# Kernel optimization log

Hardware: AMD Instinct MI355X
Metric: run time of the kernel (lower is better)

## Reference

```python
import jax, jax.numpy as jnp
import numpy as np

GROUPS = 4
KLD_SCALE = 10.0
COMMITMENT_COST = 0.25


def setup_inputs() -> dict:
    key = jax.random.key(0)
    k1, k2 = jax.random.split(key)
    z = jax.random.normal(k1, (8, 4096, 512), dtype=jnp.float32)
    embed_w = jax.random.normal(k2, (512, 128), dtype=jnp.float32)
    return {"z": z, "embed_w": embed_w}


def reference(z, embed_w):
    B, N, D = z.shape
    d = D // GROUPS  # sub-vector dim per group
    flat = z.reshape(B * N * GROUPS, d)  # [M, d]
    # squared euclidean distance to each codebook entry: [M, K]
    dist = (
        jnp.sum(flat * flat, axis=1, keepdims=True)
        - 2.0 * flat @ embed_w.T
        + jnp.sum(embed_w * embed_w, axis=1)[None, :]
    )
    ind = jnp.argmin(dist, axis=1)  # argmax(-dist)
    z_q = embed_w[ind]  # [M, d] codebook gather
    sg = jax.lax.stop_gradient
    diff = KLD_SCALE * (
        COMMITMENT_COST * jnp.mean((sg(z_q) - flat) ** 2)
        + jnp.mean((z_q - sg(flat)) ** 2)
    )
    # straight-through estimator
    z_q_st = (flat + sg(z_q - flat)).reshape(B, N, D)
    ind_out = ind.reshape(N, B, GROUPS)  # matches torch .view on contiguous buffer
    return (z_q_st, diff, ind_out)
```

## Files before the change

kernel.cpp:

```cpp
#include <hip/hip_runtime.h>
#include <float.h>


typedef _Float16 half8 __attribute__((ext_vector_type(8)));
typedef __attribute__((ext_vector_type(4))) float f32x4;

constexpr int Dn = 128;
constexpr int K  = 512;
constexpr long long Mrows = 131072;
constexpr int RPW   = 32;
constexpr int WAVES = 16;
constexpr int RPB   = RPW * WAVES;
constexpr int NBLK  = (int)(Mrows / RPB);
constexpr float TAU_A = 0.05f;

constexpr size_t ZQ_SIZE  = (size_t)Mrows * Dn;
constexpr size_t DIFF_OFF = ZQ_SIZE;
constexpr size_t IND_OFF  = ZQ_SIZE + 1;

__device__ inline void gload_lds16(const void* g, void* l) {
    __builtin_amdgcn_global_load_lds(
        (const __attribute__((address_space(1))) unsigned int*)g,
        (__attribute__((address_space(3))) unsigned int*)l,
        16, 0, 0);
}

__global__ void prep_kernel(const float* __restrict__ W,
                            unsigned short* __restrict__ Wp,
                            float* __restrict__ wn2,
                            double* __restrict__ wn64) {
    int t = blockIdx.x * 256 + threadIdx.x;
    int code = t >> 4;
    int g    = t & 15;
    const float* src = W + (size_t)code * Dn + g * 8;
    float4 a = *(const float4*)src;
    float4 b = *(const float4*)(src + 4);
    float vv[8] = {a.x, a.y, a.z, a.w, b.x, b.y, b.z, b.w};
    half8 hv;
    double s2 = 0.0;
    #pragma unroll
    for (int j = 0; j < 8; ++j) {
        hv[j] = (_Float16)vv[j];
        s2 += (double)vv[j] * (double)vv[j];
    }
    *(half8*)((char*)Wp + (size_t)code * 256 + ((g ^ (code & 7)) << 4)) = hv;
    s2 += __shfl_xor(s2, 1);
    s2 += __shfl_xor(s2, 2);
    s2 += __shfl_xor(s2, 4);
    s2 += __shfl_xor(s2, 8);
    if (g == 0) {
        wn2[code]  = (float)(-0.5 * s2);
        wn64[code] = s2;
    }
}

__global__ __launch_bounds__(1024, 4) void vq_main(
        const float* __restrict__ Z, const float* __restrict__ W,
        const unsigned short* __restrict__ Wp, const float* __restrict__ wn2,
        const double* __restrict__ wn64,
        float* __restrict__ out, double* __restrict__ diffsum) {
    __shared__ __align__(16) char Wlds[131072];
    __shared__ float wn2_s[K];
    __shared__ float xn_s[RPB];
    __shared__ int   sIdx[RPB];
    __shared__ int   flagList[RPB];
    __shared__ int   flagN;
    __shared__ float wpart[WAVES];

    const int tid  = threadIdx.x;
    const int w    = tid >> 6;
    const int lane = tid & 63;
    const int lm   = lane & 15;
    const int lg   = lane >> 4;
    const size_t row0 = (size_t)blockIdx.x * RPB;

    if (tid == 0) flagN = 0;

    {
        const char* gsrc = (const char*)Wp;
        #pragma unroll
        for (int it = 0; it < 8; ++it) {
            const int gbase = it * 1024 + w * 64;
            gload_lds16(gsrc + (size_t)(gbase + lane) * 16, Wlds + (size_t)gbase * 16);
        }
    }
    if (tid < K) wn2_s[tid] = wn2[tid];

    half8 ah[2][4];
    #pragma unroll
    for (int r = 0; r < 2; ++r) {
        const size_t grow = row0 + (size_t)w * RPW + r * 16 + lm;
        float s2 = 0.f;
        #pragma unroll
        for (int ks = 0; ks < 4; ++ks) {
            const float* xp = Z + grow * Dn + ks * 32 + lg * 8;
            float4 x0 = *(const float4*)xp;
            float4 x1 = *(const float4*)(xp + 4);
            float xv[8] = {x0.x, x0.y, x0.z, x0.w, x1.x, x1.y, x1.z, x1.w};
            #pragma unroll
            for (int j = 0; j < 8; ++j) {
                ah[r][ks][j] = (_Float16)xv[j];
                s2 += xv[j] * xv[j];
            }
        }
        s2 += __shfl_xor(s2, 16);
        s2 += __shfl_xor(s2, 32);
        if (lg == 0) xn_s[w * RPW + r * 16 + lm] = s2;
    }

    float m1[2][4], m2[2][4];
    int   i1[2][4];
    #pragma unroll
    for (int r = 0; r < 2; ++r)
        #pragma unroll
        for (int j = 0; j < 4; ++j) { m1[r][j] = -FLT_MAX; m2[r][j] = -FLT_MAX; i1[r][j] = 0; }

    asm volatile("s_waitcnt vmcnt(0)" ::: "memory");
    __syncthreads();

    const int t0 = (w * 2) & 31;
    #pragma unroll 2
    for (int ti = 0; ti < 32; ++ti) {
        const int t = (ti + t0) & 31;
        const int code = t * 16 + lm;
        const float cinit = wn2_s[code];
        half8 bh[4];
        #pragma unroll
        for (int ks = 0; ks < 4; ++ks) {
            const int off = code * 256 + ((((ks << 2) + lg) ^ (code & 7)) << 4);
            bh[ks] = *(const half8*)(Wlds + off);
        }
        f32x4 acc[2];
        #pragma unroll
        for (int r = 0; r < 2; ++r) acc[r] = (f32x4){cinit, cinit, cinit, cinit};
        #pragma unroll
        for (int ks = 0; ks < 4; ++ks) {
            #pragma unroll
            for (int r = 0; r < 2; ++r)
                acc[r] = __builtin_amdgcn_mfma_f32_16x16x32_f16(ah[r][ks], bh[ks], acc[r], 0, 0, 0);
        }
        #pragma unroll
        for (int r = 0; r < 2; ++r) {
            #pragma unroll
            for (int j = 0; j < 4; ++j) {
                const float a = acc[r][j];
                m2[r][j] = __builtin_amdgcn_fmed3f(a, m1[r][j], m2[r][j]);
                const bool gt = a > m1[r][j];
                m1[r][j] = fmaxf(m1[r][j], a);
                i1[r][j] = gt ? code : i1[r][j];
            }
        }
    }

    #pragma unroll
    for (int sft = 1; sft < 16; sft <<= 1) {
        #pragma unroll
        for (int r = 0; r < 2; ++r) {
            #pragma unroll
            for (int j = 0; j < 4; ++j) {
                float o1 = __shfl_xor(m1[r][j], sft);
                float o2 = __shfl_xor(m2[r][j], sft);
                int   oi = __shfl_xor(i1[r][j], sft);
                if (o1 > m1[r][j] || (o1 == m1[r][j] && oi < i1[r][j])) {
                    m2[r][j] = fmaxf(m1[r][j], o2);
                    m1[r][j] = o1;
                    i1[r][j] = oi;
                } else {
                    m2[r][j] = fmaxf(m2[r][j], o1);
                }
            }
        }
    }

    float psum = 0.f;
    if (lm == 0) {
        #pragma unroll
        for (int r = 0; r < 2; ++r) {
            #pragma unroll
            for (int j = 0; j < 4; ++j) {
                const int row = w * RPW + r * 16 + lg * 4 + j;
                sIdx[row] = i1[r][j];
                psum += xn_s[row] - 2.f * m1[r][j];
                if (m1[r][j] - m2[r][j] < TAU_A) {
                    int pos = atomicAdd(&flagN, 1);
                    flagList[pos] = row;
                }
            }
        }
    }
    __syncthreads();

    {
        const int nf = flagN;
        const int cg    = lane >> 3;
        const int dbase = (lane & 7) * 16;
        for (int fi = w; fi < nf; fi += WAVES) {
            const int rr = flagList[fi];
            const float* xp = Z + (row0 + rr) * Dn + dbase;
            double xd[16];
            #pragma unroll
            for (int q = 0; q < 16; q += 4) {
                float4 v = *(const float4*)(xp + q);
                xd[q] = v.x; xd[q+1] = v.y; xd[q+2] = v.z; xd[q+3] = v.w;
            }
            double best = 1e300; int bi = 0;
            for (int cb = 0; cb < 64; ++cb) {
                const int c = cb * 8 + cg;
                const float* wp = W + (size_t)c * Dn + dbase;
                double s = 0.0;
                #pragma unroll
                for (int q = 0; q < 16; q += 4) {
                    float4 wv = *(const float4*)(wp + q);
                    s += xd[q]   * (double)wv.x;
                    s += xd[q+1] * (double)wv.y;
                    s += xd[q+2] * (double)wv.z;
                    s += xd[q+3] * (double)wv.w;
                }
                s += __shfl_xor(s, 1);
                s += __shfl_xor(s, 2);
                s += __shfl_xor(s, 4);
                const double sc = wn64[c] - 2.0 * s;
                if (sc < best) { best = sc; bi = c; }
            }
            #pragma unroll
            for (int sft = 8; sft < 64; sft <<= 1) {
                double ob = __shfl_xor(best, sft);
                int    ok = __shfl_xor(bi, sft);
                if (ob < best || (ob == best && ok < bi)) { best = ob; bi = ok; }
            }
            if (lane == 0) sIdx[rr] = bi;
        }
    }
    __syncthreads();

    #pragma unroll
    for (int it = 0; it < 16; ++it) {
        int f4i = lane + it * 64;
        int rl  = f4i >> 5, cq = f4i & 31;
        int ind = sIdx[w * RPW + rl];
        float4 wv = ((const float4*)(W + (size_t)ind * Dn))[cq];
        ((float4*)(out + (row0 + w * RPW + rl) * Dn))[cq] = wv;
    }
    if (lane < RPW)
        out[IND_OFF + row0 + w * RPW + lane] = (float)sIdx[w * RPW + lane];

    #pragma unroll
    for (int sft = 1; sft < 64; sft <<= 1) psum += __shfl_xor(psum, sft);
    if (lane == 0) wpart[w] = psum;
    __syncthreads();
    if (tid == 0) {
        double t = 0.0;
        #pragma unroll
        for (int i = 0; i < WAVES; ++i) t += (double)wpart[i];
        atomicAdd(diffsum, t);
    }
}

__global__ void diff_kernel(const double* __restrict__ diffsum, float* __restrict__ out) {
    if (threadIdx.x == 0 && blockIdx.x == 0) {
        out[DIFF_OFF] = (float)(12.5 * diffsum[0] / (double)ZQ_SIZE);
    }
}

extern "C" void kernel_launch(void* const* d_in, const int* in_sizes, int n_in,
                              void* d_out, int out_size, void* d_ws, size_t ws_size,
                              hipStream_t stream) {
    (void)in_sizes; (void)n_in; (void)out_size; (void)ws_size;
    const float* Z = (const float*)d_in[0];
    const float* W = (const float*)d_in[1];
    float* out = (float*)d_out;
    double* diffsum = (double*)d_ws;
    float*  wn2  = (float*)((char*)d_ws + 64);
    double* wn64 = (double*)((char*)d_ws + 2112);
    unsigned short* Wp = (unsigned short*)((char*)d_ws + 8192);

    hipMemsetAsync(d_ws, 0, 16, stream);
    prep_kernel<<<32, 256, 0, stream>>>(W, Wp, wn2, wn64);
    vq_main<<<NBLK, 1024, 0, stream>>>(Z, W, Wp, wn2, wn64, out, diffsum);
    diff_kernel<<<1, 64, 0, stream>>>(diffsum, out);
}
```

Baseline: 113.8 us.

## Halve LDS codebook buffer and stream codebook in two staged halves

Shrinks blocks from 16 to 8 waves and replaces the full 128KB LDS codebook copy with a 64KB buffer that is filled twice, once per half of the codes, with barriers between halves. The goal is to cut per-block LDS so more blocks can be resident per CU and the codebook load is smaller per stage. In exchange it doubles the number of blocks, and so the total codebook traffic into LDS, and adds a mid-loop sync where the second half load is fully exposed rather than overlapped. It also drops the per-wave staggered start of the tile loop.

```diff
diff --git a/kernel.cpp b/kernel.cpp
--- a/kernel.cpp
+++ b/kernel.cpp
@@ -9,9 +9,10 @@
 constexpr int K  = 512;
 constexpr long long Mrows = 131072;
 constexpr int RPW   = 32;
-constexpr int WAVES = 16;
+constexpr int WAVES = 8;
 constexpr int RPB   = RPW * WAVES;
 constexpr int NBLK  = (int)(Mrows / RPB);
+constexpr int KHALF = 256;
 constexpr float TAU_A = 0.05f;
 
 constexpr size_t ZQ_SIZE  = (size_t)Mrows * Dn;
@@ -54,12 +55,12 @@
     }
 }
 
-__global__ __launch_bounds__(1024, 4) void vq_main(
+__global__ __launch_bounds__(512, 4) void vq_main(
         const float* __restrict__ Z, const float* __restrict__ W,
         const unsigned short* __restrict__ Wp, const float* __restrict__ wn2,
         const double* __restrict__ wn64,
         float* __restrict__ out, double* __restrict__ diffsum) {
-    __shared__ __align__(16) char Wlds[131072];
+    __shared__ __align__(16) char Wbuf[KHALF * 256];
     __shared__ float wn2_s[K];
     __shared__ float xn_s[RPB];
     __shared__ int   sIdx[RPB];
@@ -76,15 +77,15 @@
 
     if (tid == 0) flagN = 0;
 
-    {
-        const char* gsrc = (const char*)Wp;
+    auto stage = [&](int p) {
+        const char* gsrc = (const char*)Wp + (size_t)p * (KHALF * 256);
         #pragma unroll
         for (int it = 0; it < 8; ++it) {
-            const int gbase = it * 1024 + w * 64;
-            gload_lds16(gsrc + (size_t)(gbase + lane) * 16, Wlds + (size_t)gbase * 16);
-        }
-    }
-    if (tid < K) wn2_s[tid] = wn2[tid];
+            const int gbase = it * 512 + w * 64;
+            gload_lds16(gsrc + (size_t)(gbase + lane) * 16, Wbuf + (size_t)gbase * 16);
+        }
+    };
+    stage(0);
 
     half8 ah[2][4];
     #pragma unroll
@@ -107,6 +108,7 @@
         s2 += __shfl_xor(s2, 32);
         if (lg == 0) xn_s[w * RPW + r * 16 + lm] = s2;
     }
+    if (tid < K) wn2_s[tid] = wn2[tid];
 
     float m1[2][4], m2[2][4];
     int   i1[2][4];
@@ -118,37 +120,45 @@
     asm volatile("s_waitcnt vmcnt(0)" ::: "memory");
     __syncthreads();
 
-    const int t0 = (w * 2) & 31;
-    #pragma unroll 2
-    for (int ti = 0; ti < 32; ++ti) {
-        const int t = (ti + t0) & 31;
-        const int code = t * 16 + lm;
-        const float cinit = wn2_s[code];
-        half8 bh[4];
-        #pragma unroll
-        for (int ks = 0; ks < 4; ++ks) {
-            const int off = code * 256 + ((((ks << 2) + lg) ^ (code & 7)) << 4);
-            bh[ks] = *(const half8*)(Wlds + off);
-        }
-        f32x4 acc[2];
-        #pragma unroll
-        for (int r = 0; r < 2; ++r) acc[r] = (f32x4){cinit, cinit, cinit, cinit};
-        #pragma unroll
-        for (int ks = 0; ks < 4; ++ks) {
-            #pragma unroll
-            for (int r = 0; r < 2; ++r)
-                acc[r] = __builtin_amdgcn_mfma_f32_16x16x32_f16(ah[r][ks], bh[ks], acc[r], 0, 0, 0);
-        }
-        #pragma unroll
-        for (int r = 0; r < 2; ++r) {
-            #pragma unroll
-            for (int j = 0; j < 4; ++j) {
-                const float a = acc[r][j];
-                m2[r][j] = __builtin_amdgcn_fmed3f(a, m1[r][j], m2[r][j]);
-                const bool gt = a > m1[r][j];
-                m1[r][j] = fmaxf(m1[r][j], a);
-                i1[r][j] = gt ? code : i1[r][j];
-            }
+    for (int p = 0; p < 2; ++p) {
+        const int cbase = p * KHALF;
+        #pragma unroll 2
+        for (int t = 0; t < 16; ++t) {
+            const int code_l = t * 16 + lm;
+            const int code   = cbase + code_l;
+            const float cinit = wn2_s[code];
+            half8 bh[4];
+            #pragma unroll
+            for (int ks = 0; ks < 4; ++ks) {
+                const int off = code_l * 256 + ((((ks << 2) + lg) ^ (code_l & 7)) << 4);
+                bh[ks] = *(const half8*)(Wbuf + off);
+            }
+            f32x4 acc[2];
+            #pragma unroll
+            for (int r = 0; r < 2; ++r) acc[r] = (f32x4){cinit, cinit, cinit, cinit};
+            #pragma unroll
+            for (int ks = 0; ks < 4; ++ks) {
+                #pragma unroll
+                for (int r = 0; r < 2; ++r)
+                    acc[r] = __builtin_amdgcn_mfma_f32_16x16x32_f16(ah[r][ks], bh[ks], acc[r], 0, 0, 0);
+            }
+            #pragma unroll
+            for (int r = 0; r < 2; ++r) {
+                #pragma unroll
+                for (int j = 0; j < 4; ++j) {
+                    const float a = acc[r][j];
+                    m2[r][j] = __builtin_amdgcn_fmed3f(a, m1[r][j], m2[r][j]);
+                    const bool gt = a > m1[r][j];
+                    m1[r][j] = fmaxf(m1[r][j], a);
+                    i1[r][j] = gt ? code : i1[r][j];
+                }
+            }
+        }
+        if (p == 0) {
+            __syncthreads();
+            stage(1);
+            asm volatile("s_waitcnt vmcnt(0)" ::: "memory");
+            __syncthreads();
         }
     }
 
@@ -276,6 +286,6 @@
 
     hipMemsetAsync(d_ws, 0, 16, stream);
     prep_kernel<<<32, 256, 0, stream>>>(W, Wp, wn2, wn64);
-    vq_main<<<NBLK, 1024, 0, stream>>>(Z, W, Wp, wn2, wn64, out, diffsum);
+    vq_main<<<NBLK, 512, 0, stream>>>(Z, W, Wp, wn2, wn64, out, diffsum);
     diff_kernel<<<1, 64, 0, stream>>>(diffsum, out);
 }
```

After: 113.1 us. Within noise of the previous version (-0.6%).

## Split codebook gather into separate wide kernel and drop staggered tile order

Applied to the files above, without the earlier changes.

Moves the z_q gather and write out of the heavy 1024-thread scan kernel into a separate lightweight kernel with many small blocks. That kernel reads indices back from the output buffer and folds the final diff scalar write in through a last-block atomic counter. The intent is to keep the scan kernel's tail from serializing large stores and to spread the store traffic across more blocks. It also removes the per-wave rotated start of the codebook tile loop, which may increase LDS bank conflicts, and it adds an extra pass over the index data.

```diff
diff --git a/kernel.cpp b/kernel.cpp
--- a/kernel.cpp
+++ b/kernel.cpp
@@ -12,6 +12,8 @@
 constexpr int WAVES = 16;
 constexpr int RPB   = RPW * WAVES;
 constexpr int NBLK  = (int)(Mrows / RPB);
+constexpr int GROWS = 64;
+constexpr int NGBLK = (int)(Mrows / GROWS);
 constexpr float TAU_A = 0.05f;
 
 constexpr size_t ZQ_SIZE  = (size_t)Mrows * Dn;
@@ -54,7 +56,7 @@
     }
 }
 
-__global__ __launch_bounds__(1024, 4) void vq_main(
+__global__ __launch_bounds__(1024, 4) void vq_scan(
         const float* __restrict__ Z, const float* __restrict__ W,
         const unsigned short* __restrict__ Wp, const float* __restrict__ wn2,
         const double* __restrict__ wn64,
@@ -118,10 +120,8 @@
     asm volatile("s_waitcnt vmcnt(0)" ::: "memory");
     __syncthreads();
 
-    const int t0 = (w * 2) & 31;
     #pragma unroll 2
-    for (int ti = 0; ti < 32; ++ti) {
-        const int t = (ti + t0) & 31;
+    for (int t = 0; t < 32; ++t) {
         const int code = t * 16 + lm;
         const float cinit = wn2_s[code];
         half8 bh[4];
@@ -233,16 +233,7 @@
     }
     __syncthreads();
 
-    #pragma unroll
-    for (int it = 0; it < 16; ++it) {
-        int f4i = lane + it * 64;
-        int rl  = f4i >> 5, cq = f4i & 31;
-        int ind = sIdx[w * RPW + rl];
-        float4 wv = ((const float4*)(W + (size_t)ind * Dn))[cq];
-        ((float4*)(out + (row0 + w * RPW + rl) * Dn))[cq] = wv;
-    }
-    if (lane < RPW)
-        out[IND_OFF + row0 + w * RPW + lane] = (float)sIdx[w * RPW + lane];
+    if (tid < RPB) out[IND_OFF + row0 + tid] = (float)sIdx[tid];
 
     #pragma unroll
     for (int sft = 1; sft < 64; sft <<= 1) psum += __shfl_xor(psum, sft);
@@ -256,9 +247,27 @@
     }
 }
 
-__global__ void diff_kernel(const double* __restrict__ diffsum, float* __restrict__ out) {
-    if (threadIdx.x == 0 && blockIdx.x == 0) {
-        out[DIFF_OFF] = (float)(12.5 * diffsum[0] / (double)ZQ_SIZE);
+__global__ __launch_bounds__(256) void vq_gather(
+        const float* __restrict__ W, float* __restrict__ out,
+        const double* __restrict__ diffsum, unsigned int* __restrict__ done) {
+    __shared__ int inds[GROWS];
+    const int tid = threadIdx.x;
+    const size_t row0 = (size_t)blockIdx.x * GROWS;
+    if (tid < GROWS) inds[tid] = (int)out[IND_OFF + row0 + tid];
+    __syncthreads();
+    #pragma unroll
+    for (int it = 0; it < 8; ++it) {
+        int f4i = tid + it * 256;
+        int rl  = f4i >> 5, cq = f4i & 31;
+        int ind = inds[rl];
+        float4 wv = ((const float4*)(W + (size_t)ind * Dn))[cq];
+        ((float4*)(out + (row0 + rl) * Dn))[cq] = wv;
+    }
+    if (tid == 0) {
+        unsigned int old = atomicAdd(done, 1u);
+        if (old == (unsigned int)(NGBLK - 1)) {
+            out[DIFF_OFF] = (float)(12.5 * diffsum[0] / (double)ZQ_SIZE);
+        }
     }
 }
 
@@ -270,12 +279,13 @@
     const float* W = (const float*)d_in[1];
     float* out = (float*)d_out;
     double* diffsum = (double*)d_ws;
+    unsigned int* done = (unsigned int*)((char*)d_ws + 8);
     float*  wn2  = (float*)((char*)d_ws + 64);
     double* wn64 = (double*)((char*)d_ws + 2112);
     unsigned short* Wp = (unsigned short*)((char*)d_ws + 8192);
 
     hipMemsetAsync(d_ws, 0, 16, stream);
     prep_kernel<<<32, 256, 0, stream>>>(W, Wp, wn2, wn64);
-    vq_main<<<NBLK, 1024, 0, stream>>>(Z, W, Wp, wn2, wn64, out, diffsum);
-    diff_kernel<<<1, 64, 0, stream>>>(diffsum, out);
-}
+    vq_scan<<<NBLK, 1024, 0, stream>>>(Z, W, Wp, wn2, wn64, out, diffsum);
+    vq_gather<<<NGBLK, 256, 0, stream>>>(W, out, diffsum, done);
+}
```

After: 134.8 us. +18.5%, slower.
